# Performance work log

Measured on AMD Instinct MI355X. Metric: run time of the kernel, lower is better.

## Reference

```python
import jax, jax.numpy as jnp
import numpy as np

TOKENS, IN_F, OUT_F = 8192, 4096, 4096
INPUT_ZERO_POINT = 3  # Z_x, baked into shifted_q_bias at quantization time
QMIN, QMAX = -128, 127  # 8-bit signed range


def setup_inputs() -> dict:
    key = jax.random.key(0)
    k1, k2, k3, k4 = jax.random.split(key, 4)
    # int8-valued quantized activations and per-output-channel symmetric int8 weights
    q_x = jax.random.randint(k1, (TOKENS, IN_F), -128, 128, dtype=jnp.int32)
    q_weight = jax.random.randint(k2, (OUT_F, IN_F), -127, 128, dtype=jnp.int32)
    # per-output-channel weight scale (symmetric per-channel quantization)
    weight_scale = jax.random.uniform(k3, (OUT_F,), minval=1e-3, maxval=1e-2, dtype=jnp.float32)
    # int32 quantized bias; shifted by the input zero-point correction term:
    # shifted_q_bias = q_bias - Z_x * q_W.sum(dim=1)
    q_bias = jax.random.randint(k4, (OUT_F,), -(2 ** 15), 2 ** 15, dtype=jnp.int32)
    shifted_q_bias = q_bias - INPUT_ZERO_POINT * jnp.sum(q_weight, axis=1, dtype=jnp.int32)
    return {
        "q_x": q_x,
        "q_weight": q_weight,
        "shifted_q_bias": shifted_q_bias,
        "weight_scale": weight_scale,
        "input_scale": jnp.float32(0.02),
        "output_scale": jnp.float32(0.05),
        "output_zero_point": jnp.float32(-5.0),
    }


def reference(q_x, q_weight, shifted_q_bias, weight_scale, input_scale, output_scale, output_zero_point):
    # GPU path of get_matmul_quantized_output: float-cast int GEMM with fused bias
    acc = jnp.dot(q_x.astype(jnp.float32), q_weight.T.astype(jnp.float32))
    acc = acc + shifted_q_bias.astype(jnp.float32)  # [tokens, out]
    # per-output-channel requant scale: S_W * S_X / S_Y
    scale = weight_scale * input_scale / output_scale  # [out]
    y = scale * acc + output_zero_point
    return jnp.clip(jnp.round(y), QMIN, QMAX).astype(jnp.int8)
```

## Files before the change

kernel.cpp:

```cpp
#include <hip/hip_runtime.h>

#define TOKENS 8192
#define IN_F   4096
#define OUT_F  4096

#define BM 256
#define BN 256
#define BKB 128
#define NT (IN_F / BKB)
#define NI (NT / 2)

using int4v = __attribute__((ext_vector_type(4))) int;
typedef __attribute__((address_space(3))) char       lds_char_t;
typedef const __attribute__((address_space(1))) char glob_char_t;

__global__ void pack_i32_to_i8(const int* __restrict__ src, int* __restrict__ dst, int n4) {
    int stride = gridDim.x * blockDim.x;
    for (int i = blockIdx.x * blockDim.x + threadIdx.x; i < n4; i += stride) {
        int4v v = ((const int4v*)src)[i];
        dst[i] = (v.x & 0xff) | ((v.y & 0xff) << 8) | ((v.z & 0xff) << 16) | (v.w << 24);
    }
}

__global__ __launch_bounds__(512, 2) void qgemm_i8(
    const signed char* __restrict__ A,
    const signed char* __restrict__ Bw,
    const int*   __restrict__ bias,
    const float* __restrict__ wscale,
    const float* __restrict__ p_si, const float* __restrict__ p_so, const float* __restrict__ p_zp,
    int* __restrict__ C)
{
    constexpr int N = OUT_F, K = IN_F;
    constexpr int NBN = N / BN;

    __shared__ __align__(16) signed char smem[131072];

    int nwg = gridDim.x, bid = blockIdx.x, swz = bid;
    if ((nwg & 7) == 0) { int cpx = nwg >> 3; swz = (bid & 7) * cpx + (bid >> 3); }
    int bm = swz / NBN, bn = swz - bm * NBN;

    const int t = threadIdx.x, wid = t >> 6, l = t & 63;
    const int wr = wid >> 2, wc = wid & 3, lr = l & 15, lg = l >> 4;

    const int k0off = ((lg       ^ (lr & 7)) << 4);
    const int k1off = (((4 + lg) ^ (lr & 7)) << 4);
    const int arow = (wr * 128 + lr) * 128;
    const int brow = (wc * 64  + lr) * 128;

    const int srow = t >> 3;
    const int scol = (((t & 7) ^ ((t >> 3) & 7)) << 4);
    const signed char* gApl = A  + (size_t)(bm * BM + srow) * K + scol;
    const signed char* gBpl = Bw + (size_t)(bn * BN + srow) * K + scol;

#define STA(bufOff_, h_, tt_) do {                                                                 \
    __builtin_amdgcn_global_load_lds((glob_char_t*)(gApl + (size_t)((h_)*128      ) * K + (tt_)*BKB), \
        (lds_char_t*)smem + (bufOff_) + (h_)*16384 +        wid*1024, 16, 0, 0);                   \
    __builtin_amdgcn_global_load_lds((glob_char_t*)(gApl + (size_t)((h_)*128 + 64 ) * K + (tt_)*BKB), \
        (lds_char_t*)smem + (bufOff_) + (h_)*16384 + 8192 + wid*1024, 16, 0, 0);                   \
} while (0)
#define STB(bufOff_, h_, tt_) do {                                                                 \
    __builtin_amdgcn_global_load_lds((glob_char_t*)(gBpl + (size_t)((h_)*128      ) * K + (tt_)*BKB), \
        (lds_char_t*)smem + (bufOff_) + 32768 + (h_)*16384 +        wid*1024, 16, 0, 0);           \
    __builtin_amdgcn_global_load_lds((glob_char_t*)(gBpl + (size_t)((h_)*128 + 64 ) * K + (tt_)*BKB), \
        (lds_char_t*)smem + (bufOff_) + 32768 + (h_)*16384 + 8192 + wid*1024, 16, 0, 0);           \
} while (0)

#define LDA4(bufOff_, mb_) do { _Pragma("unroll") for (int mm = 0; mm < 4; ++mm) {                 \
    a[(mb_)+mm][0] = *(const int4v*)(smem + (bufOff_) + arow + ((mb_)+mm)*2048 + k0off);           \
    a[(mb_)+mm][1] = *(const int4v*)(smem + (bufOff_) + arow + ((mb_)+mm)*2048 + k1off); } } while (0)
#define LDB2(bufOff_, nb_) do { _Pragma("unroll") for (int nn = 0; nn < 2; ++nn) {                 \
    b[(nb_)+nn][0] = *(const int4v*)(smem + (bufOff_) + 32768 + brow + ((nb_)+nn)*2048 + k0off);   \
    b[(nb_)+nn][1] = *(const int4v*)(smem + (bufOff_) + 32768 + brow + ((nb_)+nn)*2048 + k1off); } } while (0)

#define MF(mb_, nb_) do { _Pragma("unroll") for (int kk = 0; kk < 2; ++kk)                         \
    _Pragma("unroll") for (int mm = 0; mm < 4; ++mm)                                               \
    _Pragma("unroll") for (int nn = 0; nn < 2; ++nn)                                               \
        acc[(mb_)+mm][(nb_)+nn] = __builtin_amdgcn_mfma_i32_16x16x64_i8(                           \
            a[(mb_)+mm][kk], b[(nb_)+nn][kk], acc[(mb_)+mm][(nb_)+nn], 0, 0, 0); } while (0)

#define PH_MID() do { __builtin_amdgcn_s_barrier(); __builtin_amdgcn_s_setprio(1); } while (0)
#define PH_END() do { __builtin_amdgcn_s_setprio(0); __builtin_amdgcn_s_barrier(); } while (0)

    int4v acc[8][4] = {};
    int4v a[8][2], b[4][2];

    STA(0, 0, 0); STA(0, 1, 0); STB(0, 0, 0); STB(0, 1, 0);
    STA(65536, 0, 1); STA(65536, 1, 1);
    asm volatile("s_waitcnt vmcnt(4)" ::: "memory");
    __builtin_amdgcn_s_barrier();

#define ITER(i_, FULL_) do {                                                                       \
    const int t1 = 2*(i_)+1, t2 = 2*(i_)+2, t3 = 2*(i_)+3;                                         \
     LDB2(0, 0); LDA4(0, 0); STB(65536, 0, t1);                                            \
    PH_MID(); MF(0, 0); PH_END();                                                                  \
     LDA4(0, 4); STB(65536, 1, t1);                                                        \
    PH_MID(); MF(4, 0); PH_END();                                                                  \
     LDB2(0, 2); if (FULL_) STA(0, 0, t2);                                                 \
    PH_MID(); MF(0, 2); PH_END();                                                                  \
     if (FULL_) STA(0, 1, t2);                                                             \
    PH_MID(); MF(4, 2); __builtin_amdgcn_s_setprio(0);                                             \
    if (FULL_) { asm volatile("s_waitcnt vmcnt(4)" ::: "memory"); }                                \
    else       { asm volatile("s_waitcnt vmcnt(0)" ::: "memory"); }                                \
    __builtin_amdgcn_s_barrier();                                                                  \
     LDB2(65536, 0); LDA4(65536, 0); if (FULL_) STB(0, 0, t2);                             \
    PH_MID(); MF(0, 0); PH_END();                                                                  \
     LDA4(65536, 4); if (FULL_) STB(0, 1, t2);                                             \
    PH_MID(); MF(4, 0); PH_END();                                                                  \
     LDB2(65536, 2); if (FULL_) STA(65536, 0, t3);                                         \
    PH_MID(); MF(0, 2); PH_END();                                                                  \
     if (FULL_) STA(65536, 1, t3);                                                         \
    PH_MID(); MF(4, 2); __builtin_amdgcn_s_setprio(0);                                             \
    if (FULL_) { asm volatile("s_waitcnt vmcnt(4)" ::: "memory"); }                                \
    __builtin_amdgcn_s_barrier();                                                                  \
} while (0)

    for (int i = 0; i < NI - 1; ++i) ITER(i, 1);
    ITER(NI - 1, 0);

#undef ITER
#undef PH_END
#undef PH_MID
#undef MF
#undef LDB2
#undef LDA4
#undef STB
#undef STA

    float si = p_si[0], so = p_so[0], z = p_zp[0];
    float rs = si / so;

    #pragma unroll
    for (int n = 0; n < 4; ++n) {
        int col = bn * BN + wc * 64 + n * 16 + lr;
        float sc = wscale[col] * rs;
        int   bs = bias[col];
        #pragma unroll
        for (int m = 0; m < 8; ++m) {
            int row = bm * BM + wr * 128 + m * 16 + lg * 4;
            #pragma unroll
            for (int r = 0; r < 4; ++r) {
                float y = sc * (float)(acc[m][n][r] + bs) + z;
                y = rintf(y);
                y = fminf(fmaxf(y, -128.0f), 127.0f);
                C[(size_t)(row + r) * N + col] = (int)y;
            }
        }
    }
}

__global__ void qgemm_naive(const int* __restrict__ qx, const int* __restrict__ qw,
                            const int* __restrict__ bias, const float* __restrict__ wscale,
                            const float* __restrict__ si, const float* __restrict__ so,
                            const float* __restrict__ zp, int* __restrict__ out) {
    int idx = blockIdx.x * blockDim.x + threadIdx.x;
    if (idx >= TOKENS * OUT_F) return;
    int row = idx / OUT_F, col = idx - row * OUT_F;
    const int4v* xa = (const int4v*)(qx + (size_t)row * IN_F);
    const int4v* wb = (const int4v*)(qw + (size_t)col * IN_F);
    int acc = 0;
    for (int k = 0; k < IN_F / 4; ++k) {
        int4v a = xa[k], b = wb[k];
        acc += a.x * b.x + a.y * b.y + a.z * b.z + a.w * b.w;
    }
    float y = wscale[col] * si[0] / so[0] * (float)(acc + bias[col]) + zp[0];
    y = fminf(fmaxf(rintf(y), -128.0f), 127.0f);
    out[idx] = (int)y;
}

extern "C" void kernel_launch(void* const* d_in, const int* in_sizes, int n_in,
                              void* d_out, int out_size, void* d_ws, size_t ws_size,
                              hipStream_t stream) {
    const int*   q_x    = (const int*)d_in[0];
    const int*   q_w    = (const int*)d_in[1];
    const int*   bias   = (const int*)d_in[2];
    const float* wscale = (const float*)d_in[3];
    const float* s_in   = (const float*)d_in[4];
    const float* s_out  = (const float*)d_in[5];
    const float* zp     = (const float*)d_in[6];
    int* out = (int*)d_out;

    const size_t needA = (size_t)TOKENS * IN_F;
    const size_t needB = (size_t)OUT_F * IN_F;

    if (ws_size >= needA + needB) {
        signed char* pA = (signed char*)d_ws;
        signed char* pB = pA + needA;
        pack_i32_to_i8<<<2048, 256, 0, stream>>>(q_x, (int*)pA, (int)(needA / 4));
        pack_i32_to_i8<<<1024, 256, 0, stream>>>(q_w, (int*)pB, (int)(needB / 4));
        int grid = (TOKENS / BM) * (OUT_F / BN);
        qgemm_i8<<<grid, 512, 0, stream>>>(pA, pB, bias, wscale, s_in, s_out, zp, out);
    } else {
        int total = TOKENS * OUT_F;
        qgemm_naive<<<(total + 255) / 256, 256, 0, stream>>>(q_x, q_w, bias, wscale, s_in, s_out, zp, out);
    }
}
```

Before: 183.8 us.

## Software-pipeline LDS fragment loads one phase ahead of MFMA and halve barriers

Restructures the main K loop so the LDS register loads for the next phase are issued alongside the current phase's MFMA block. This replaces the two barriers per phase with a single one, and the vmcnt waits move earlier into the phase. The aim is to hide LDS read latency behind matrix math and cut synchronisation overhead. It adds register pressure, because a/b fragments are consumed while the next ones load, and it changes the hazard ordering between buffer overwrites and reads.

```diff
diff --git a/kernel.cpp b/kernel.cpp
--- a/kernel.cpp
+++ b/kernel.cpp
@@ -78,48 +78,52 @@
         acc[(mb_)+mm][(nb_)+nn] = __builtin_amdgcn_mfma_i32_16x16x64_i8(                           \
             a[(mb_)+mm][kk], b[(nb_)+nn][kk], acc[(mb_)+mm][(nb_)+nn], 0, 0, 0); } while (0)
 
-#define PH_MID() do { __builtin_amdgcn_s_barrier(); __builtin_amdgcn_s_setprio(1); } while (0)
-#define PH_END() do { __builtin_amdgcn_s_setprio(0); __builtin_amdgcn_s_barrier(); } while (0)
+#define SP1 __builtin_amdgcn_s_setprio(1)
+#define SP0 __builtin_amdgcn_s_setprio(0)
+#define BAR __builtin_amdgcn_s_barrier()
+#define VM(n_) asm volatile("s_waitcnt vmcnt(" #n_ ")" ::: "memory")
 
     int4v acc[8][4] = {};
     int4v a[8][2], b[4][2];
 
     STA(0, 0, 0); STA(0, 1, 0); STB(0, 0, 0); STB(0, 1, 0);
     STA(65536, 0, 1); STA(65536, 1, 1);
-    asm volatile("s_waitcnt vmcnt(4)" ::: "memory");
-    __builtin_amdgcn_s_barrier();
-
-#define ITER(i_, FULL_) do {                                                                       \
+    VM(4);
+    BAR;
+    LDB2(0, 0); LDA4(0, 0);
+
+#define ITER_FULL(i_) do {                                                                         \
     const int t1 = 2*(i_)+1, t2 = 2*(i_)+2, t3 = 2*(i_)+3;                                         \
-     LDB2(0, 0); LDA4(0, 0); STB(65536, 0, t1);                                            \
-    PH_MID(); MF(0, 0); PH_END();                                                                  \
-     LDA4(0, 4); STB(65536, 1, t1);                                                        \
-    PH_MID(); MF(4, 0); PH_END();                                                                  \
-     LDB2(0, 2); if (FULL_) STA(0, 0, t2);                                                 \
-    PH_MID(); MF(0, 2); PH_END();                                                                  \
-     if (FULL_) STA(0, 1, t2);                                                             \
-    PH_MID(); MF(4, 2); __builtin_amdgcn_s_setprio(0);                                             \
-    if (FULL_) { asm volatile("s_waitcnt vmcnt(4)" ::: "memory"); }                                \
-    else       { asm volatile("s_waitcnt vmcnt(0)" ::: "memory"); }                                \
-    __builtin_amdgcn_s_barrier();                                                                  \
-     LDB2(65536, 0); LDA4(65536, 0); if (FULL_) STB(0, 0, t2);                             \
-    PH_MID(); MF(0, 0); PH_END();                                                                  \
-     LDA4(65536, 4); if (FULL_) STB(0, 1, t2);                                             \
-    PH_MID(); MF(4, 0); PH_END();                                                                  \
-     LDB2(65536, 2); if (FULL_) STA(65536, 0, t3);                                         \
-    PH_MID(); MF(0, 2); PH_END();                                                                  \
-     if (FULL_) STA(65536, 1, t3);                                                         \
-    PH_MID(); MF(4, 2); __builtin_amdgcn_s_setprio(0);                                             \
-    if (FULL_) { asm volatile("s_waitcnt vmcnt(4)" ::: "memory"); }                                \
-    __builtin_amdgcn_s_barrier();                                                                  \
-} while (0)
-
-    for (int i = 0; i < NI - 1; ++i) ITER(i, 1);
-    ITER(NI - 1, 0);
-
-#undef ITER
-#undef PH_END
-#undef PH_MID
+     STB(65536, 0, t1); LDA4(0, 4);                  SP1; MF(0, 0); SP0;        BAR;         \
+     STB(65536, 1, t1); LDB2(0, 2);                  SP1; MF(4, 0); SP0;        BAR;         \
+     STA(0, 0, t2);                                  SP1; MF(0, 2); SP0; VM(2); BAR;         \
+     STA(0, 1, t2);     LDB2(65536, 0); LDA4(65536, 0); SP1; MF(4, 2); SP0;     BAR;         \
+     STB(0, 0, t2);     LDA4(65536, 4);              SP1; MF(0, 0); SP0;        BAR;         \
+     STB(0, 1, t2);     LDB2(65536, 2);              SP1; MF(4, 0); SP0;        BAR;         \
+     STA(65536, 0, t3);                              SP1; MF(0, 2); SP0; VM(2); BAR;         \
+     STA(65536, 1, t3); LDB2(0, 0); LDA4(0, 0);      SP1; MF(4, 2); SP0;        BAR;         \
+} while (0)
+
+#define ITER_TAIL() do {                                                                           \
+     STB(65536, 0, 31); LDA4(0, 4);                  SP1; MF(0, 0); SP0;        BAR;         \
+     STB(65536, 1, 31); LDB2(0, 2);                  SP1; MF(4, 0); SP0;        BAR;         \
+                                                     SP1; MF(0, 2); SP0; VM(0); BAR;         \
+     LDB2(65536, 0); LDA4(65536, 0);                 SP1; MF(4, 2); SP0;        BAR;         \
+     LDA4(65536, 4);                                 SP1; MF(0, 0); SP0;        BAR;         \
+     LDB2(65536, 2);                                 SP1; MF(4, 0); SP0;        BAR;         \
+                                                     SP1; MF(0, 2); SP0;        BAR;         \
+                                                     SP1; MF(4, 2); SP0;                     \
+} while (0)
+
+    for (int i = 0; i < NI - 1; ++i) ITER_FULL(i);
+    ITER_TAIL();
+
+#undef ITER_TAIL
+#undef ITER_FULL
+#undef VM
+#undef BAR
+#undef SP0
+#undef SP1
 #undef MF
 #undef LDB2
 #undef LDA4
```

After: 181.6 us. About the same (-1.2%).
